# Kernel tuning notes

Measured on AMD Instinct MI355X. Metric: run time of the kernel, lower is better.

The kernel has to match this reference:

```python
import jax, jax.numpy as jnp
import numpy as np

T = 0.1  # temperature
NEG_M = 1.0


def _normalize(v):
    return v / jnp.linalg.norm(v, axis=1, keepdims=True)


def setup_inputs() -> dict:
    key = jax.random.key(0)
    k1, k2 = jax.random.split(key)
    f1 = _normalize(jax.random.normal(k1, (4096, 128), dtype=jnp.float32))
    f2 = _normalize(jax.random.normal(k2, (4096, 128), dtype=jnp.float32))
    return {"f1": f1, "f2": f2, "dd": 1}


def reference(f1, f2, dd):
    # x: [N, D] with N = 2*B; dd is unused (matches original forward)
    x = jnp.concatenate([f1, f2], axis=0)
    N = x.shape[0]
    half = N // 2
    # positive pairs: (i, i+half) and (i+half, i)
    reordered = jnp.concatenate([x[half:], x[:half]], axis=0)
    # original uses .data (detached) on the second operand
    pos = jnp.exp(jnp.sum(x * jax.lax.stop_gradient(reordered), axis=1) / T)  # [N]
    sim = jnp.matmul(x, jax.lax.stop_gradient(x.T)) / T                       # [N, N]
    diag_mask = 1.0 - jnp.eye(N, dtype=x.dtype)
    all_prob = jnp.exp(sim) * diag_mask                                        # [N, N]
    all_div = all_prob.sum(axis=1)                                             # [N]
    lnPmt = pos / all_div                                                      # P(pos)
    Pon = all_prob / all_div[:, None]
    # sum_j log(1 - P_ij) minus the positive-pair term log(1 - P_pos)
    lnPon = jnp.log1p(-Pon).sum(axis=1) - jnp.log1p(-lnPmt)                    # [N]
    lnPmtsum = jnp.log(lnPmt).sum()
    lnPonsum = lnPon.sum() * NEG_M
    loss = -(lnPmtsum + lnPonsum) / N
    return loss
```

## Files before the change

### kernel.cpp

```cpp
#include <hip/hip_runtime.h>
#include <hip/hip_bf16.h>
#include <hip/hip_fp8.h>

#define HALF 4096
#define NTOT 8192
#define D 128
#define KS2 3.79828256f

typedef __attribute__((ext_vector_type(4))) float f32x4;

__device__ __forceinline__ float wave_sum64(float v) {
#pragma unroll
    for (int m = 32; m >= 1; m >>= 1) v += __shfl_xor(v, m);
    return v;
}

__global__ void cast_pos_kernel(const float* __restrict__ f1, const float* __restrict__ f2,
                                unsigned char* __restrict__ xs, float* __restrict__ spos,
                                float* __restrict__ sii2, float* __restrict__ acc,
                                unsigned int* __restrict__ done) {
    if (blockIdx.x == 0 && threadIdx.x == 0) { *acc = 0.f; *done = 0u; }

    int w = (blockIdx.x * blockDim.x + threadIdx.x) >> 6;
    int l = threadIdx.x & 63;
    float2 a1 = ((const float2*)(f1 + (size_t)w * D))[l];
    float2 a2 = ((const float2*)(f2 + (size_t)w * D))[l];

    __hip_fp8_e4m3 q1x(a1.x * KS2), q1y(a1.y * KS2);
    __hip_fp8_e4m3 q2x(a2.x * KS2), q2y(a2.y * KS2);

    int g = w >> 4, lrow = w & 15;
    int k = l >> 4, quad = (l >> 2) & 3, j = (l & 3) * 2;
    size_t off = (size_t)g * 2048 + k * 512 + (quad * 16 + lrow) * 8 + j;
    *(unsigned short*)(xs + off) =
        (unsigned short)(q1x.__x | ((unsigned short)q1y.__x << 8));
    *(unsigned short*)(xs + off + 256 * 2048) =
        (unsigned short)(q2x.__x | ((unsigned short)q2y.__x << 8));

    float b1x = (float)q1x, b1y = (float)q1y;
    float b2x = (float)q2x, b2y = (float)q2y;
    float s1 = b1x * b1x + b1y * b1y;
    float s2 = b2x * b2x + b2y * b2y;
    float d  = a1.x * a2.x + a1.y * a2.y;
    s1 = wave_sum64(s1); s2 = wave_sum64(s2); d = wave_sum64(d);
    if (l == 0) {
        sii2[w] = s1; sii2[w + HALF] = s2;
        float sp = d * 10.0f;
        spos[w] = sp; spos[w + HALF] = sp;
    }
}

__global__ __launch_bounds__(256, 4) void gram_kernel(const unsigned char* __restrict__ xs,
                                                      float* __restrict__ E1p) {
    const int slab = blockIdx.x;
    const int panel = blockIdx.y;
    const int t = threadIdx.x;
    const int wave = t >> 6, lane = t & 63;
    const int lrow = lane & 15, quad = lane >> 4;

    const unsigned char* ab = xs + (size_t)panel * 4 * 2048 + lane * 8;
    long af[4][4];
#pragma unroll
    for (int k = 0; k < 4; ++k)
#pragma unroll
        for (int r = 0; r < 4; ++r)
            af[k][r] = *(const long*)(ab + r * 2048 + k * 512);

    const unsigned char* bb = xs + ((size_t)slab * 64 + wave * 2) * 2048 + lane * 8;
    long bfr[4][2];
#pragma unroll
    for (int k = 0; k < 4; ++k)
#pragma unroll
        for (int c = 0; c < 2; ++c)
            bfr[k][c] = *(const long*)(bb + c * 2048 + k * 512);

    f32x4 rs4[4];
#pragma unroll
    for (int r = 0; r < 4; ++r) rs4[r] = (f32x4){0.f, 0.f, 0.f, 0.f};

#pragma unroll 1
    for (int tt = 0; tt < 8; ++tt) {
        f32x4 a2[4][2];
#pragma unroll
        for (int r = 0; r < 4; ++r)
#pragma unroll
            for (int c = 0; c < 2; ++c) a2[r][c] = (f32x4){0.f, 0.f, 0.f, 0.f};
#pragma unroll
        for (int k = 0; k < 4; ++k)
#pragma unroll
            for (int r = 0; r < 4; ++r)
#pragma unroll
                for (int c = 0; c < 2; ++c)
                    a2[r][c] = __builtin_amdgcn_mfma_f32_16x16x32_fp8_fp8(af[k][r], bfr[k][c], a2[r][c], 0, 0, 0);

        if (tt < 7) {
            const unsigned char* bn = bb + (size_t)(tt + 1) * 8 * 2048;
#pragma unroll
            for (int k = 0; k < 4; ++k)
#pragma unroll
                for (int c = 0; c < 2; ++c)
                    bfr[k][c] = *(const long*)(bn + c * 2048 + k * 512);
        }

#pragma unroll
        for (int r = 0; r < 4; ++r)
#pragma unroll
            for (int c = 0; c < 2; ++c)
#pragma unroll
                for (int g = 0; g < 4; ++g)
                    rs4[r][g] += __builtin_amdgcn_exp2f(a2[r][c][g]);
    }

    const int slot = slab * 4 + wave;
#pragma unroll
    for (int r = 0; r < 4; ++r) {
#pragma unroll
        for (int g = 0; g < 4; ++g) {
            float v = rs4[r][g];
#pragma unroll
            for (int m = 1; m <= 8; m <<= 1) v += __shfl_xor(v, m);
            if (lrow == 0)
                E1p[(size_t)slot * NTOT + panel * 64 + r * 16 + quad * 4 + g] = v;
        }
    }
}

__global__ void rowterm_kernel(const float* __restrict__ E1p, const float* __restrict__ spos,
                               const float* __restrict__ sii2, float* __restrict__ acc,
                               unsigned int* __restrict__ done, float* __restrict__ out) {
    int i = blockIdx.x * 256 + threadIdx.x;
    float div = 0.f;
#pragma unroll
    for (int s = 0; s < 32; ++s) div += E1p[(size_t)s * NTOT + i];
    div -= __builtin_amdgcn_exp2f(sii2[i]);
    float sp = spos[i];
    float pmt = __expf(sp) / div;
    float term = sp - __logf(div) - 1.0f - __logf(1.0f - pmt);

    term = wave_sum64(term);
    __shared__ float red[4];
    if ((threadIdx.x & 63) == 0) red[threadIdx.x >> 6] = term;
    __syncthreads();
    if (threadIdx.x == 0) {
        atomicAdd(acc, red[0] + red[1] + red[2] + red[3]);
        __threadfence();
        unsigned int prev = atomicAdd(done, 1u);
        if (prev == 31u) {
            float total = atomicAdd(acc, 0.0f);
            out[0] = -total * (1.0f / (float)NTOT);
        }
    }
}

extern "C" void kernel_launch(void* const* d_in, const int* in_sizes, int n_in,
                              void* d_out, int out_size, void* d_ws, size_t ws_size,
                              hipStream_t stream) {
    const float* f1 = (const float*)d_in[0];
    const float* f2 = (const float*)d_in[1];
    float* out = (float*)d_out;

    char* ws = (char*)d_ws;
    unsigned char* xs = (unsigned char*)ws;
    float* E1p  = (float*)(ws + (size_t)NTOT * D);
    float* spos = E1p + 32 * NTOT;
    float* sii2 = spos + NTOT;
    float* acc  = sii2 + NTOT;
    unsigned int* done = (unsigned int*)(acc + 1);

    cast_pos_kernel<<<1024, 256, 0, stream>>>(f1, f2, xs, spos, sii2, acc, done);
    gram_kernel<<<dim3(8, 128), 256, 0, stream>>>(xs, E1p);
    rowterm_kernel<<<32, 256, 0, stream>>>(E1p, spos, sii2, acc, done, out);
}
```

Before: 80.18 us.

## Fuse row-term reduction into gram kernel via per-panel last-block completion counters

```diff
diff --git a/kernel.cpp b/kernel.cpp
--- a/kernel.cpp
+++ b/kernel.cpp
@@ -18,8 +18,12 @@
 __global__ void cast_pos_kernel(const float* __restrict__ f1, const float* __restrict__ f2,
                                 unsigned char* __restrict__ xs, float* __restrict__ spos,
                                 float* __restrict__ sii2, float* __restrict__ acc,
-                                unsigned int* __restrict__ done) {
-    if (blockIdx.x == 0 && threadIdx.x == 0) { *acc = 0.f; *done = 0u; }
+                                unsigned int* __restrict__ done,
+                                unsigned int* __restrict__ pdone) {
+    if (blockIdx.x == 0) {
+        if (threadIdx.x == 0) { *acc = 0.f; *done = 0u; }
+        if (threadIdx.x < 128) pdone[threadIdx.x] = 0u;
+    }
 
     int w = (blockIdx.x * blockDim.x + threadIdx.x) >> 6;
     int l = threadIdx.x & 63;
@@ -51,7 +55,13 @@
 }
 
 __global__ __launch_bounds__(256, 4) void gram_kernel(const unsigned char* __restrict__ xs,
-                                                      float* __restrict__ E1p) {
+                                                      float* __restrict__ E1p,
+                                                      const float* __restrict__ spos,
+                                                      const float* __restrict__ sii2,
+                                                      float* __restrict__ acc,
+                                                      unsigned int* __restrict__ done,
+                                                      unsigned int* __restrict__ pdone,
+                                                      float* __restrict__ out) {
     const int slab = blockIdx.x;
     const int panel = blockIdx.y;
     const int t = threadIdx.x;
@@ -123,31 +133,34 @@
                 E1p[(size_t)slot * NTOT + panel * 64 + r * 16 + quad * 4 + g] = v;
         }
     }
-}
 
-__global__ void rowterm_kernel(const float* __restrict__ E1p, const float* __restrict__ spos,
-                               const float* __restrict__ sii2, float* __restrict__ acc,
-                               unsigned int* __restrict__ done, float* __restrict__ out) {
-    int i = blockIdx.x * 256 + threadIdx.x;
-    float div = 0.f;
+    __threadfence();
+    __syncthreads();
+    __shared__ int winner;
+    if (t == 0) winner = (atomicAdd(&pdone[panel], 1u) == 7u) ? 1 : 0;
+    __syncthreads();
+    if (!winner) return;
+    __threadfence();
+
+    if (t < 64) {
+        int i = panel * 64 + t;
+        float div = 0.f;
 #pragma unroll
-    for (int s = 0; s < 32; ++s) div += E1p[(size_t)s * NTOT + i];
-    div -= __builtin_amdgcn_exp2f(sii2[i]);
-    float sp = spos[i];
-    float pmt = __expf(sp) / div;
-    float term = sp - __logf(div) - 1.0f - __logf(1.0f - pmt);
+        for (int s = 0; s < 32; ++s) div += E1p[(size_t)s * NTOT + i];
+        div -= __builtin_amdgcn_exp2f(sii2[i]);
+        float sp = spos[i];
+        float pmt = __expf(sp) / div;
+        float term = sp - __logf(div) - 1.0f - __logf(1.0f - pmt);
 
-    term = wave_sum64(term);
-    __shared__ float red[4];
-    if ((threadIdx.x & 63) == 0) red[threadIdx.x >> 6] = term;
-    __syncthreads();
-    if (threadIdx.x == 0) {
-        atomicAdd(acc, red[0] + red[1] + red[2] + red[3]);
-        __threadfence();
-        unsigned int prev = atomicAdd(done, 1u);
-        if (prev == 31u) {
-            float total = atomicAdd(acc, 0.0f);
-            out[0] = -total * (1.0f / (float)NTOT);
+        term = wave_sum64(term);
+        if (t == 0) {
+            atomicAdd(acc, term);
+            __threadfence();
+            unsigned int prev = atomicAdd(done, 1u);
+            if (prev == 127u) {
+                float total = atomicAdd(acc, 0.0f);
+                out[0] = -total * (1.0f / (float)NTOT);
+            }
         }
     }
 }
@@ -165,9 +178,9 @@
     float* spos = E1p + 32 * NTOT;
     float* sii2 = spos + NTOT;
     float* acc  = sii2 + NTOT;
-    unsigned int* done = (unsigned int*)(acc + 1);
+    unsigned int* done  = (unsigned int*)(acc + 1);
+    unsigned int* pdone = done + 1;
 
-    cast_pos_kernel<<<1024, 256, 0, stream>>>(f1, f2, xs, spos, sii2, acc, done);
-    gram_kernel<<<dim3(8, 128), 256, 0, stream>>>(xs, E1p);
-    rowterm_kernel<<<32, 256, 0, stream>>>(E1p, spos, sii2, acc, done, out);
+    cast_pos_kernel<<<1024, 256, 0, stream>>>(f1, f2, xs, spos, sii2, acc, done, pdone);
+    gram_kernel<<<dim3(8, 128), 256, 0, stream>>>(xs, E1p, spos, sii2, acc, done, pdone, out);
 }
```

New measurement: 181.0 us. +125.7%, slower.
